# Kernel tuning notes

Hardware: AMD Instinct MI355X
Metric: run time of the kernel (lower is better)

The kernel has to match this reference:

```python
import jax, jax.numpy as jnp
import numpy as np
import math

D_MODEL = 1024
DK = 64
N_HEADS = 16
B, S = 8, 1024


def setup_inputs() -> dict:
    key = jax.random.key(0)
    ks = jax.random.split(key, 9)
    scale_in = 1.0 / math.sqrt(D_MODEL)
    scale_cat = 1.0 / math.sqrt(N_HEADS * DK)
    x = jax.random.normal(ks[0], (B, S, D_MODEL), dtype=jnp.float32)
    # per-head stacked weights: [H, D, dk]
    Wq = jax.random.uniform(ks[1], (N_HEADS, D_MODEL, DK), jnp.float32, -scale_in, scale_in)
    bq = jax.random.uniform(ks[2], (N_HEADS, DK), jnp.float32, -scale_in, scale_in)
    Wk = jax.random.uniform(ks[3], (N_HEADS, D_MODEL, DK), jnp.float32, -scale_in, scale_in)
    bk = jax.random.uniform(ks[4], (N_HEADS, DK), jnp.float32, -scale_in, scale_in)
    Wv = jax.random.uniform(ks[5], (N_HEADS, D_MODEL, DK), jnp.float32, -scale_in, scale_in)
    bv = jax.random.uniform(ks[6], (N_HEADS, DK), jnp.float32, -scale_in, scale_in)
    Wo = jax.random.uniform(ks[7], (N_HEADS * DK, DK), jnp.float32, -scale_cat, scale_cat)
    bo = jax.random.uniform(ks[8], (DK,), jnp.float32, -scale_cat, scale_cat)
    return {"input_vector": x, "Wq": Wq, "bq": bq, "Wk": Wk, "bk": bk,
            "Wv": Wv, "bv": bv, "Wo": Wo, "bo": bo}


def reference(input_vector, Wq, bq, Wk, bk, Wv, bv, Wo, bo):
    # per-head linear projections + ReLU (heads batched via einsum)
    # q/k/v: [B, H, S, dk]
    q = jax.nn.relu(jnp.einsum('bsd,hdk->bhsk', input_vector, Wq) + bq[None, :, None, :])
    k = jax.nn.relu(jnp.einsum('bsd,hdk->bhsk', input_vector, Wk) + bk[None, :, None, :])
    v = jax.nn.relu(jnp.einsum('bsd,hdk->bhsk', input_vector, Wv) + bv[None, :, None, :])
    # raw attention scores (returned unscaled, like the torch module's `att`)
    att = jnp.einsum('bhqk,bhsk->bhqs', q, k)  # [B, H, S, S]
    probs = jax.nn.softmax(att / math.sqrt(DK), axis=-1)
    heads = jnp.einsum('bhqs,bhsk->bhqk', probs, v)  # [B, H, S, dk]
    # concat heads along feature dim: [B, S, H*dk]
    z = heads.transpose(0, 2, 1, 3).reshape(heads.shape[0], heads.shape[2], -1)
    z_out = jax.nn.relu(z @ Wo + bo)
    return (z_out, att)
```

## Files before the change

kernel.cpp:

```cpp
#include <hip/hip_runtime.h>


typedef __bf16 bf16x8 __attribute__((ext_vector_type(8)));
typedef float f32x4 __attribute__((ext_vector_type(4)));
typedef unsigned short u16x8 __attribute__((ext_vector_type(8)));
typedef unsigned short u16x4 __attribute__((ext_vector_type(4)));

typedef __attribute__((address_space(1))) unsigned int as1_u32;
typedef __attribute__((address_space(3))) unsigned int as3_u32;

#define MFMA16(a, b, c) __builtin_amdgcn_mfma_f32_16x16x32_bf16(a, b, c, 0, 0, 0)

__device__ __forceinline__ void gload_lds16(const void* g, void* l) {
  __builtin_amdgcn_global_load_lds((const as1_u32*)g, (as3_u32*)l, 16, 0, 0);
}

__device__ __forceinline__ unsigned short f2bf(float f) {
  union { float f; unsigned u; } a; a.f = f;
  unsigned r = a.u + 0x7FFFu + ((a.u >> 16) & 1u);
  return (unsigned short)(r >> 16);
}

__global__ __launch_bounds__(256) void pack_all(const float* __restrict__ x, const float* __restrict__ Wq,
                                                const float* __restrict__ Wk, const float* __restrict__ Wv,
                                                const float* __restrict__ Wo, const float* __restrict__ bq,
                                                const float* __restrict__ bk, const float* __restrict__ bv,
                                                ushort* __restrict__ xb, ushort* __restrict__ Wp,
                                                ushort* __restrict__ Wop, float* __restrict__ bqkv) {
  const int bid = blockIdx.x;
  if (bid < 8192) {
    const size_t i = ((size_t)bid * 256 + threadIdx.x) * 4;
    const float4 v = *(const float4*)(x + i);
    u16x4 o; o[0] = f2bf(v.x); o[1] = f2bf(v.y); o[2] = f2bf(v.z); o[3] = f2bf(v.w);
    *(u16x4*)(xb + i) = o;
  } else if (bid < 20480) {
    const int b2 = bid - 8192;
    const int swz = (b2 & 7) * 1536 + (b2 >> 3);
    const int o = swz * 256 + threadIdx.x;
    const int n = o >> 10, d = o & 1023;
    const int proj = n >> 10, hk = n & 1023;
    const float* W = proj == 0 ? Wq : (proj == 1 ? Wk : Wv);
    const int h = hk >> 6, kk = hk & 63;
    Wp[o] = f2bf(W[((size_t)h * 1024 + d) * 64 + kk]);
  } else {
    const int idx = (bid - 20480) * 256 + threadIdx.x;
    if (idx < 65536) {
      const int n = idx >> 10, c = idx & 1023;
      Wop[idx] = f2bf(Wo[c * 64 + n]);
    } else if (idx < 65536 + 3072) {
      const int n = idx - 65536;
      const int proj = n >> 10;
      const float* bb = proj == 0 ? bq : (proj == 1 ? bk : bv);
      bqkv[n] = bb[n & 1023];
    }
  }
}

__global__ __launch_bounds__(256) void gemm_qkv(const ushort* __restrict__ xb, const ushort* __restrict__ Wp,
                                                const float* __restrict__ bqkv, ushort* __restrict__ qo,
                                                ushort* __restrict__ ko, ushort* __restrict__ vTo) {
  __shared__ ushort As[128 * 32], Bs[128 * 32];
  const int bid = blockIdx.x;
  const int swz = (bid & 7) * 192 + (bid >> 3);
  const int by = swz / 24, bx = swz - by * 24;
  const int t = threadIdx.x, w = t >> 6, l = t & 63, lg = l >> 4, lr = l & 15;
  const int m0 = by * 128, n0 = bx * 128;
  const int wm = w >> 1, wn = w & 1;
  const int srow = l >> 2, sslot = l & 3;
  f32x4 acc[4][4] = {};
  for (int kt = 0; kt < 32; ++kt) {
    __syncthreads();
#pragma unroll
    for (int c = 0; c < 2; ++c) {
      const int cc = w * 2 + c;
      const int row = cc * 16 + srow;
      gload_lds16(xb + (size_t)(m0 + row) * 1024 + kt * 32 + sslot * 8, &As[cc * 512]);
      gload_lds16(Wp + (size_t)(n0 + row) * 1024 + kt * 32 + sslot * 8, &Bs[cc * 512]);
    }
    __syncthreads();
    bf16x8 af[4], bfr[4];
#pragma unroll
    for (int mt = 0; mt < 4; ++mt)
      af[mt] = *(const bf16x8*)(&As[(wm * 64 + mt * 16 + lr) * 32 + lg * 8]);
#pragma unroll
    for (int nt = 0; nt < 4; ++nt)
      bfr[nt] = *(const bf16x8*)(&Bs[(wn * 64 + nt * 16 + lr) * 32 + lg * 8]);
#pragma unroll
    for (int mt = 0; mt < 4; ++mt)
#pragma unroll
      for (int nt = 0; nt < 4; ++nt)
        acc[mt][nt] = MFMA16(af[mt], bfr[nt], acc[mt][nt]);
  }
#pragma unroll
  for (int nt = 0; nt < 4; ++nt) {
    const int n = n0 + wn * 64 + nt * 16 + lr;
    const float bias = bqkv[n];
    const int proj = n >> 10, h = (n >> 6) & 15, dk = n & 63;
#pragma unroll
    for (int mt = 0; mt < 4; ++mt) {
      const int mb = m0 + wm * 64 + mt * 16 + lg * 4;
      const int b = mb >> 10, s = mb & 1023;
      float vv[4];
#pragma unroll
      for (int j = 0; j < 4; ++j) {
        float a = acc[mt][nt][j] + bias;
        vv[j] = a > 0.f ? a : 0.f;
      }
      if (proj == 2) {
        u16x4 o; o[0] = f2bf(vv[0]); o[1] = f2bf(vv[1]); o[2] = f2bf(vv[2]); o[3] = f2bf(vv[3]);
        *(u16x4*)(vTo + ((size_t)(b * 16 + h) * 64 + dk) * 1024 + s) = o;
      } else {
        ushort* op = proj == 0 ? qo : ko;
#pragma unroll
        for (int j = 0; j < 4; ++j)
          op[((size_t)(b * 16 + h) * 1024 + s + j) * 64 + dk] = f2bf(vv[j]);
      }
    }
  }
}

__global__ __launch_bounds__(256) void attn_kernel(const ushort* __restrict__ qg, const ushort* __restrict__ kg,
                                                   const ushort* __restrict__ vT, float* __restrict__ att,
                                                   ushort* __restrict__ heads) {
  const int bid = blockIdx.x;
  const int swz = (bid & 7) * 256 + (bid >> 3);
  const int qt = swz & 15, bh = swz >> 4;
  const int t = threadIdx.x, w = t >> 6, l = t & 63;
  const int lg = l >> 4, lr = l & 15;
  __shared__ ushort Ks[128 * 64];
  __shared__ ushort Vs[64 * 128];
  __shared__ ushort p_q[4][16][40];
  __shared__ float s_st[4][16][40];

  const ushort* qb = qg + (size_t)bh * 65536;
  const ushort* kb = kg + (size_t)bh * 65536;
  const ushort* vb = vT + (size_t)bh * 65536;
  const int qrow0 = qt * 64 + w * 16;

  const bf16x8 qf0 = *(const bf16x8*)(qb + (qrow0 + lr) * 64 + lg * 8);
  const bf16x8 qf1 = *(const bf16x8*)(qb + (qrow0 + lr) * 64 + 32 + lg * 8);

  const int krow = l >> 3, kch = l & 7;
  const int vrow = l >> 4, vch = l & 15;
  const int frow = l >> 3, fcol = (l & 7) * 4;

  const float C2 = 0.125f * 1.44269504f;
  f32x4 oacc[4] = {};
  float lsum = 0.f;
  float* attw = att + ((size_t)bh * 1024 + qrow0) * 1024;

  for (int g = 0; g < 8; ++g) {
    const int kv0 = g * 128;
    __syncthreads();
#pragma unroll
    for (int c2 = 0; c2 < 4; ++c2) {
      const int call = w * 4 + c2;
      const int r = call * 8 + krow;
      gload_lds16(kb + (size_t)(kv0 + r) * 64 + ((kch ^ (r & 7)) * 8), &Ks[call * 512]);
      const int rv = call * 4 + vrow;
      gload_lds16(vb + (size_t)rv * 1024 + kv0 + ((vch ^ (rv & 15)) * 8), &Vs[call * 512]);
    }
    __syncthreads();
    f32x4 sf[8];
#pragma unroll
    for (int f = 0; f < 8; ++f) {
      const int r = f * 16 + lr;
      const bf16x8 kf0 = *(const bf16x8*)(&Ks[r * 64 + ((lg ^ (r & 7)) * 8)]);
      const bf16x8 kf1 = *(const bf16x8*)(&Ks[r * 64 + (((4 + lg) ^ (r & 7)) * 8)]);
      f32x4 s = {};
      s = MFMA16(kf0, qf0, s);
      s = MFMA16(kf1, qf1, s);
      sf[f] = s;
    }
#pragma unroll
    for (int s = 0; s < 4; ++s) {
#pragma unroll
      for (int fi = 0; fi < 2; ++fi) {
        const int f = 2 * s + fi;
        u16x4 pk;
#pragma unroll
        for (int j = 0; j < 4; ++j) {
          const float p = exp2f(sf[f][j] * C2);
          lsum += p;
          pk[j] = f2bf(p);
        }
        *(u16x4*)(&p_q[w][lr][fi * 16 + lg * 4]) = pk;
        *(f32x4*)(&s_st[w][lr][fi * 16 + lg * 4]) = sf[f];
      }
      asm volatile("s_waitcnt lgkmcnt(0)" ::: "memory");
      __builtin_amdgcn_sched_barrier(0);
      const bf16x8 pa = *(const bf16x8*)(&p_q[w][lr][lg * 8]);
#pragma unroll
      for (int i = 0; i < 2; ++i) {
        const int r = i * 8 + frow;
        const f32x4 fv = *(const f32x4*)(&s_st[w][r][fcol]);
        __builtin_nontemporal_store(fv,
            (f32x4*)(attw + (size_t)r * 1024 + kv0 + s * 32 + fcol));
      }
#pragma unroll
      for (int nt = 0; nt < 4; ++nt) {
        const int r = nt * 16 + lr;
        const bf16x8 vf = *(const bf16x8*)(&Vs[r * 128 + (((s * 4 + lg) ^ lr) * 8)]);
        oacc[nt] = MFMA16(pa, vf, oacc[nt]);
      }
    }
  }
  lsum += __shfl_xor(lsum, 16, 64);
  lsum += __shfl_xor(lsum, 32, 64);
  float rdiv[4];
#pragma unroll
  for (int j = 0; j < 4; ++j) rdiv[j] = 1.f / __shfl(lsum, lg * 4 + j, 16);
  const int b = bh >> 4, h = bh & 15;
#pragma unroll
  for (int nt = 0; nt < 4; ++nt)
#pragma unroll
    for (int j = 0; j < 4; ++j)
      __builtin_nontemporal_store(f2bf(oacc[nt][j] * rdiv[j]),
          heads + (size_t)(b * 1024 + qrow0 + lg * 4 + j) * 1024 + h * 64 + nt * 16 + lr);
}

__global__ __launch_bounds__(256) void gemm_out(const ushort* __restrict__ z, const ushort* __restrict__ Wop,
                                                const float* __restrict__ bo, float* __restrict__ out) {
  __shared__ float red[2][16][64];
  const int t = threadIdx.x, w = t >> 6, l = t & 63, lg = l >> 4, lr = l & 15;
  const int wm = w & 1, kh = w >> 1;
  const int m0 = blockIdx.x * 32 + wm * 16;
  f32x4 acc[4] = {};
  for (int kk = kh * 16; kk < kh * 16 + 16; ++kk) {
    bf16x8 af = *(const bf16x8*)(z + (size_t)(m0 + lr) * 1024 + kk * 32 + lg * 8);
#pragma unroll
    for (int nt = 0; nt < 4; ++nt) {
      bf16x8 bfr = *(const bf16x8*)(Wop + (size_t)(nt * 16 + lr) * 1024 + kk * 32 + lg * 8);
      acc[nt] = MFMA16(af, bfr, acc[nt]);
    }
  }
  if (kh == 1) {
#pragma unroll
    for (int nt = 0; nt < 4; ++nt)
#pragma unroll
      for (int j = 0; j < 4; ++j) red[wm][lg * 4 + j][nt * 16 + lr] = acc[nt][j];
  }
  __syncthreads();
  if (kh == 0) {
#pragma unroll
    for (int nt = 0; nt < 4; ++nt) {
      const int n = nt * 16 + lr;
      const float bb = bo[n];
#pragma unroll
      for (int j = 0; j < 4; ++j) {
        const int m = m0 + lg * 4 + j;
        float vv = acc[nt][j] + red[wm][lg * 4 + j][n] + bb;
        out[(size_t)m * 64 + n] = vv > 0.f ? vv : 0.f;
      }
    }
  }
}

extern "C" void kernel_launch(void* const* d_in, const int* in_sizes, int n_in,
                              void* d_out, int out_size, void* d_ws, size_t ws_size,
                              hipStream_t stream) {
  const float* x  = (const float*)d_in[0];
  const float* Wq = (const float*)d_in[1];
  const float* bq = (const float*)d_in[2];
  const float* Wk = (const float*)d_in[3];
  const float* bk = (const float*)d_in[4];
  const float* Wv = (const float*)d_in[5];
  const float* bv = (const float*)d_in[6];
  const float* Wo = (const float*)d_in[7];
  const float* bo = (const float*)d_in[8];
  float* out = (float*)d_out;
  float* att = out + 524288;

  char* ws = (char*)d_ws;
  size_t off = 0;
  ushort* xb  = (ushort*)(ws + off); off += (size_t)8192 * 1024 * 2;
  ushort* Wp  = (ushort*)(ws + off); off += (size_t)3072 * 1024 * 2;
  ushort* Wop = (ushort*)(ws + off); off += (size_t)64 * 1024 * 2;
  float* bqkv = (float*)(ws + off);  off += (size_t)3072 * 4;
  ushort* q   = (ushort*)(ws + off); off += (size_t)128 * 1024 * 64 * 2;
  ushort* k   = (ushort*)(ws + off); off += (size_t)128 * 1024 * 64 * 2;
  ushort* vT  = (ushort*)(ws + off); off += (size_t)128 * 64 * 1024 * 2;
  ushort* hds = (ushort*)(ws + off); off += (size_t)8192 * 1024 * 2;
  (void)ws_size; (void)in_sizes; (void)n_in; (void)out_size;

  pack_all<<<dim3(20749), dim3(256), 0, stream>>>(x, Wq, Wk, Wv, Wo, bq, bk, bv,
                                                  xb, Wp, Wop, bqkv);
  gemm_qkv<<<dim3(1536), dim3(256), 0, stream>>>(xb, Wp, bqkv, q, k, vT);
  attn_kernel<<<dim3(2048), dim3(256), 0, stream>>>(q, k, vT, att, hds);
  gemm_out<<<dim3(256), dim3(256), 0, stream>>>(hds, Wop, bo, out);
}
```

Measured before the change: 229.1 us.

## Double-buffer K/V tiles in attention and use plain stores for scores

```diff
diff --git a/kernel.cpp b/kernel.cpp
--- a/kernel.cpp
+++ b/kernel.cpp
@@ -127,8 +127,8 @@
   const int qt = swz & 15, bh = swz >> 4;
   const int t = threadIdx.x, w = t >> 6, l = t & 63;
   const int lg = l >> 4, lr = l & 15;
-  __shared__ ushort Ks[128 * 64];
-  __shared__ ushort Vs[64 * 128];
+  __shared__ ushort Ks[2][64 * 64];
+  __shared__ ushort Vs[2][64 * 64];
   __shared__ ushort p_q[4][16][40];
   __shared__ float s_st[4][16][40];
 
@@ -141,7 +141,6 @@
   const bf16x8 qf1 = *(const bf16x8*)(qb + (qrow0 + lr) * 64 + 32 + lg * 8);
 
   const int krow = l >> 3, kch = l & 7;
-  const int vrow = l >> 4, vch = l & 15;
   const int frow = l >> 3, fcol = (l & 7) * 4;
 
   const float C2 = 0.125f * 1.44269504f;
@@ -149,31 +148,39 @@
   float lsum = 0.f;
   float* attw = att + ((size_t)bh * 1024 + qrow0) * 1024;
 
-  for (int g = 0; g < 8; ++g) {
-    const int kv0 = g * 128;
-    __syncthreads();
-#pragma unroll
-    for (int c2 = 0; c2 < 4; ++c2) {
-      const int call = w * 4 + c2;
-      const int r = call * 8 + krow;
-      gload_lds16(kb + (size_t)(kv0 + r) * 64 + ((kch ^ (r & 7)) * 8), &Ks[call * 512]);
-      const int rv = call * 4 + vrow;
-      gload_lds16(vb + (size_t)rv * 1024 + kv0 + ((vch ^ (rv & 15)) * 8), &Vs[call * 512]);
-    }
-    __syncthreads();
-    f32x4 sf[8];
-#pragma unroll
-    for (int f = 0; f < 8; ++f) {
+#define ATTN_STAGE(bufi, gi)                                                      \
+  do {                                                                            \
+    const int kv0s = (gi) * 64;                                                   \
+    _Pragma("unroll")                                                             \
+    for (int c2 = 0; c2 < 2; ++c2) {                                              \
+      const int call = w * 2 + c2;                                                \
+      const int rr = call * 8 + krow;                                             \
+      gload_lds16(kb + (size_t)(kv0s + rr) * 64 + ((kch ^ (rr & 7)) * 8),         \
+                  &Ks[bufi][call * 512]);                                         \
+      gload_lds16(vb + (size_t)rr * 1024 + kv0s + ((kch ^ (rr & 7)) * 8),         \
+                  &Vs[bufi][call * 512]);                                         \
+    }                                                                             \
+  } while (0)
+
+  ATTN_STAGE(0, 0);
+  __syncthreads();
+  for (int g = 0; g < 16; ++g) {
+    const int kv0 = g * 64;
+    const int buf = g & 1;
+    if (g < 15) ATTN_STAGE(buf ^ 1, g + 1);
+    f32x4 sf[4];
+#pragma unroll
+    for (int f = 0; f < 4; ++f) {
       const int r = f * 16 + lr;
-      const bf16x8 kf0 = *(const bf16x8*)(&Ks[r * 64 + ((lg ^ (r & 7)) * 8)]);
-      const bf16x8 kf1 = *(const bf16x8*)(&Ks[r * 64 + (((4 + lg) ^ (r & 7)) * 8)]);
+      const bf16x8 kf0 = *(const bf16x8*)(&Ks[buf][r * 64 + ((lg ^ (r & 7)) * 8)]);
+      const bf16x8 kf1 = *(const bf16x8*)(&Ks[buf][r * 64 + (((4 + lg) ^ (r & 7)) * 8)]);
       f32x4 s = {};
       s = MFMA16(kf0, qf0, s);
       s = MFMA16(kf1, qf1, s);
       sf[f] = s;
     }
 #pragma unroll
-    for (int s = 0; s < 4; ++s) {
+    for (int s = 0; s < 2; ++s) {
 #pragma unroll
       for (int fi = 0; fi < 2; ++fi) {
         const int f = 2 * s + fi;
@@ -194,17 +201,18 @@
       for (int i = 0; i < 2; ++i) {
         const int r = i * 8 + frow;
         const f32x4 fv = *(const f32x4*)(&s_st[w][r][fcol]);
-        __builtin_nontemporal_store(fv,
-            (f32x4*)(attw + (size_t)r * 1024 + kv0 + s * 32 + fcol));
+        *(f32x4*)(attw + (size_t)r * 1024 + kv0 + s * 32 + fcol) = fv;
       }
 #pragma unroll
       for (int nt = 0; nt < 4; ++nt) {
         const int r = nt * 16 + lr;
-        const bf16x8 vf = *(const bf16x8*)(&Vs[r * 128 + (((s * 4 + lg) ^ lr) * 8)]);
+        const bf16x8 vf = *(const bf16x8*)(&Vs[buf][r * 64 + (((s * 4 + lg) ^ (r & 7)) * 8)]);
         oacc[nt] = MFMA16(pa, vf, oacc[nt]);
       }
     }
-  }
+    __syncthreads();
+  }
+#undef ATTN_STAGE
   lsum += __shfl_xor(lsum, 16, 64);
   lsum += __shfl_xor(lsum, 32, 64);
   float rdiv[4];
```

After: 303.6 us. +32.6%, slower.
